# Optimization experiments

Measured on AMD Instinct MI355X. Metric: run time of the kernel, lower is better.

Reference implementation:

```python
import jax, jax.numpy as jnp
import numpy as np
import math

D_MODEL = 1024
N_HEADS = 16
D_HEAD = D_MODEL // N_HEADS


def _pos_encoding(seq_len, d_model):
    # matches get_pos_encoding: paired frequencies (repeat_interleave(2)),
    # sin on even columns, cos on odd columns of the SAME angle matrix.
    position = jnp.arange(seq_len, dtype=jnp.float32)[:, None]          # [L,1]
    div = 1.0 / (10000.0 ** (jnp.arange(0, d_model, 2, dtype=jnp.float32) / d_model))
    div = jnp.repeat(div, 2)[None, :]                                    # [1,D]
    ang = position * div                                                 # [L,D]
    col = jnp.arange(d_model)
    return jnp.where(col[None, :] % 2 == 0, jnp.sin(ang), jnp.cos(ang))


def _rel_enc_shift(a):
    # a: [b, h, l, m] -> Transformer-XL relative shift
    b, h, l, m = a.shape
    a = jnp.concatenate([a, jnp.zeros((b, h, l, 1), a.dtype)], axis=-1)  # [b,h,l,m+1]
    a = a.reshape(b, h, l * (m + 1))
    a = a[:, :, l - 1: l - 1 + l * m]
    return a.reshape(b, h, l, m)


def setup_inputs() -> dict:
    key = jax.random.key(0)
    ks = jax.random.split(key, 10)
    B, S, D = 1, 2048, D_MODEL
    s = 1.0 / math.sqrt(D)
    inp = {
        "query": jax.random.normal(ks[0], (B, S, D), jnp.float32),
        "key": jax.random.normal(ks[1], (B, S, D), jnp.float32),
        "value": jax.random.normal(ks[2], (B, S, D), jnp.float32),
        "attn_mask": jnp.zeros((1, 1, S, S), jnp.float32),
        "Wq": jax.random.normal(ks[3], (D, D), jnp.float32) * s,
        "Wke": jax.random.normal(ks[4], (D, D), jnp.float32) * s,
        "Wkr": jax.random.normal(ks[5], (D, D), jnp.float32) * s,
        "Wv": jax.random.normal(ks[6], (D, D), jnp.float32) * s,
        "Wf": jax.random.normal(ks[7], (D, D), jnp.float32) * s,
        "u_param": jax.random.normal(ks[8], (1, 1, N_HEADS, D_HEAD), jnp.float32),
        "v_param": jax.random.normal(ks[9], (1, 1, N_HEADS, D_HEAD), jnp.float32),
    }
    return inp


def reference(query, key, value, attn_mask, Wq, Wke, Wkr, Wv, Wf, u_param, v_param):
    B, S, D = query.shape
    F = key.shape[1]
    H, dh = u_param.shape[2], u_param.shape[3]
    sqrt_dk = math.sqrt(D)

    rel_enc = _pos_encoding(F, D)[::-1, :]                     # flipped along seq dim

    q = (query @ Wq.T).reshape(B, S, H, dh)
    k = (key @ Wke.T).reshape(B, F, H, dh)
    v = (value @ Wv.T).reshape(B, F, H, dh)

    A_C = jnp.einsum('bsnd,bfnd->bnsf', q + u_param, k)
    Q = (rel_enc @ Wkr.T).reshape(F, H, dh)
    B_D_hat = jnp.einsum('bsnd,fnd->bnsf', q + v_param, Q)
    B_D = _rel_enc_shift(B_D_hat)

    score = (A_C + B_D) / sqrt_dk + attn_mask
    weights = jax.nn.softmax(score, axis=-1)                   # [B,H,S,F]
    attention_loss = jnp.mean(jnp.max(weights, axis=(-1, -2)))

    out = jnp.einsum('bnsf,bfnd->bsnd', weights, v).reshape(B, S, D)
    out = jax.nn.gelu(out @ Wf.T, approximate=False)
    return out, weights, attention_loss
```

## Files before the change

kernel.cpp:

```cpp
#include <hip/hip_runtime.h>
#include <math.h>

#define SEQ 2048
#define DMODEL 1024
#define NHEADS 16
#define DHEAD 64

#define LSLOTS 64
#define LSTRIDE 32

typedef long long i64;
typedef unsigned short u16;
typedef __attribute__((ext_vector_type(4))) float f32x4;
typedef __attribute__((ext_vector_type(8))) short bf16x8;

#define IN_E  2097152
#define W_E   1048576
#define HEAD_E 131072

__device__ inline u16 f2bf(float x) {
    union { float f; unsigned u; } v; v.f = x;
    unsigned r = v.u + 0x7FFF + ((v.u >> 16) & 1);
    return (u16)(r >> 16);
}
__device__ inline float bf2f(u16 h) {
    union { unsigned u; float f; } v; v.u = ((unsigned)h) << 16;
    return v.f;
}

__device__ inline void gload16(const void* g, void* l) {
    __builtin_amdgcn_global_load_lds(
        (const __attribute__((address_space(1))) unsigned int*)g,
        (__attribute__((address_space(3))) unsigned int*)l, 16, 0, 0);
}

struct SplitArgs {
    const float* src[8];
    u16* dh[8];
    u16* dl[8];
    int n4[8];
};
__global__ __launch_bounds__(256)
void split_all(SplitArgs a)
{
    const int z = blockIdx.y;
    const int i = blockIdx.x * 256 + threadIdx.x;
    if (i >= a.n4[z]) return;
    const float4 x = ((const float4*)a.src[z])[i];
    u16 h0 = f2bf(x.x), h1 = f2bf(x.y), h2 = f2bf(x.z), h3 = f2bf(x.w);
    u16 l0 = f2bf(x.x - bf2f(h0)), l1 = f2bf(x.y - bf2f(h1));
    u16 l2 = f2bf(x.z - bf2f(h2)), l3 = f2bf(x.w - bf2f(h3));
    uint2 hh; hh.x = (unsigned)h0 | ((unsigned)h1 << 16); hh.y = (unsigned)h2 | ((unsigned)h3 << 16);
    uint2 ll; ll.x = (unsigned)l0 | ((unsigned)l1 << 16); ll.y = (unsigned)l2 | ((unsigned)l3 << 16);
    ((uint2*)a.dh[z])[i] = hh;
    ((uint2*)a.dl[z])[i] = ll;
}

__global__ __launch_bounds__(256)
void posenc_split(u16* __restrict__ dh, u16* __restrict__ dl)
{
    const int idx = blockIdx.x * 256 + threadIdx.x;
    const int f = idx >> 10;
    const int i = idx & 1023;
    const float P = (float)(SEQ - 1 - f);
    const float ex = (float)(i & ~1) * (1.f / 1024.f);
    const float dv = powf(10000.f, -ex);
    const float ang = P * dv;
    const float val = (i & 1) ? cosf(ang) : sinf(ang);
    const u16 hb = f2bf(val);
    dh[idx] = hb;
    dl[idx] = f2bf(val - bf2f(hb));
}

struct TNArgs {
    const u16 *Ah, *Al, *Bh, *Bl;
    i64 sAz, sBz;
    float* Cf; i64 sCz; int ldc;
    u16 *O1h, *O1l, *O2h, *O2l;
    const float *b1, *b2;
    int K, mode;
};

__global__ __launch_bounds__(256)
void mfma_tn128(TNArgs p)
{
    __shared__ __align__(16) u16 Ash[128 * 32];
    __shared__ __align__(16) u16 Asl[128 * 32];
    __shared__ __align__(16) u16 Bsh[128 * 32];
    __shared__ __align__(16) u16 Bsl[128 * 32];
    const int tid = threadIdx.x, wave = tid >> 6, lane = tid & 63;
    const int z = blockIdx.z;
    const i64 m0 = (i64)blockIdx.y * 128, n0 = (i64)blockIdx.x * 128;
    const int K = p.K;
    const u16* Abh = p.Ah + (i64)z * p.sAz;
    const u16* Abl = p.Al + (i64)z * p.sAz;
    const u16* Bbh = p.Bh + (i64)z * p.sBz;
    const u16* Bbl = p.Bl + (i64)z * p.sBz;
    const int r0 = tid >> 2, kc = (tid & 3) * 8;
    const int r1 = r0 + 64;
    u16* dA0 = &Ash[wave * 512];
    u16* dA1 = &Ash[2048 + wave * 512];
    u16* dA0l = &Asl[wave * 512];
    u16* dA1l = &Asl[2048 + wave * 512];
    u16* dB0 = &Bsh[wave * 512];
    u16* dB1 = &Bsh[2048 + wave * 512];
    u16* dB0l = &Bsl[wave * 512];
    u16* dB1l = &Bsl[2048 + wave * 512];
    const int wm = (wave >> 1) * 64, wn = (wave & 1) * 64;
    f32x4 acc[4][4] = {};

    for (int k0 = 0; k0 < K; k0 += 32) {
        __syncthreads();
        const i64 ga0 = (m0 + r0) * K + k0 + kc;
        const i64 ga1 = (m0 + r1) * K + k0 + kc;
        const i64 gb0 = (n0 + r0) * K + k0 + kc;
        const i64 gb1 = (n0 + r1) * K + k0 + kc;
        gload16(Abh + ga0, dA0);  gload16(Abh + ga1, dA1);
        gload16(Abl + ga0, dA0l); gload16(Abl + ga1, dA1l);
        gload16(Bbh + gb0, dB0);  gload16(Bbh + gb1, dB1);
        gload16(Bbl + gb0, dB0l); gload16(Bbl + gb1, dB1l);
        __syncthreads();
        const int fr = lane & 15, fk = (lane >> 4) * 8;
        bf16x8 fah[4], fal[4], fbh[4], fbl[4];
#pragma unroll
        for (int t = 0; t < 4; ++t) {
            fah[t] = *(const bf16x8*)&Ash[(wm + t * 16 + fr) * 32 + fk];
            fal[t] = *(const bf16x8*)&Asl[(wm + t * 16 + fr) * 32 + fk];
            fbh[t] = *(const bf16x8*)&Bsh[(wn + t * 16 + fr) * 32 + fk];
            fbl[t] = *(const bf16x8*)&Bsl[(wn + t * 16 + fr) * 32 + fk];
        }
#pragma unroll
        for (int mi = 0; mi < 4; ++mi)
#pragma unroll
            for (int ni = 0; ni < 4; ++ni) {
                acc[mi][ni] = __builtin_amdgcn_mfma_f32_16x16x32_bf16(fah[mi], fbh[ni], acc[mi][ni], 0, 0, 0);
                acc[mi][ni] = __builtin_amdgcn_mfma_f32_16x16x32_bf16(fah[mi], fbl[ni], acc[mi][ni], 0, 0, 0);
                acc[mi][ni] = __builtin_amdgcn_mfma_f32_16x16x32_bf16(fal[mi], fbh[ni], acc[mi][ni], 0, 0, 0);
            }
    }

    const int fr = lane & 15, fq = (lane >> 4) * 4;
    if (p.mode == 0) {
        float* C = p.Cf + (i64)z * p.sCz;
#pragma unroll
        for (int mi = 0; mi < 4; ++mi)
#pragma unroll
            for (int e = 0; e < 4; ++e) {
                const i64 row = m0 + wm + mi * 16 + fq + e;
#pragma unroll
                for (int ni = 0; ni < 4; ++ni)
                    C[row * p.ldc + n0 + wn + ni * 16 + fr] = acc[mi][ni][e];
            }
    } else if (p.mode == 3) {
        float* C = p.Cf + (i64)z * p.sCz;
#pragma unroll
        for (int mi = 0; mi < 4; ++mi)
#pragma unroll
            for (int e = 0; e < 4; ++e) {
                const int r = (int)(m0 + wm + mi * 16 + fq + e);
#pragma unroll
                for (int ni = 0; ni < 4; ++ni) {
                    const int f = (int)n0 + wn + ni * 16 + fr;
                    if (f >= SEQ - 1 - r)
                        C[(i64)r * SEQ + (f + r - (SEQ - 1))] = acc[mi][ni][e];
                    else if (r >= 1)
                        C[(i64)(r - 1) * SEQ + (f + r + 1)] = acc[mi][ni][e];
                }
            }
    } else if (p.mode == 1) {
        const i64 obase = (i64)z * IN_E;
#pragma unroll
        for (int mi = 0; mi < 4; ++mi)
#pragma unroll
            for (int e = 0; e < 4; ++e) {
                const i64 m = m0 + wm + mi * 16 + fq + e;
#pragma unroll
                for (int ni = 0; ni < 4; ++ni) {
                    const int c = (int)n0 + wn + ni * 16 + fr;
                    const int h = c >> 6, d = c & 63;
                    const i64 off = ((i64)h * SEQ + m) * DHEAD + d;
                    float v = acc[mi][ni][e];
                    if (z == 0) v += p.b1[c];
                    const u16 hb = f2bf(v);
                    const u16 lb = f2bf(v - bf2f(hb));
                    p.O1h[obase + off] = hb;
                    p.O1l[obase + off] = lb;
                    if (z == 0) {
                        const float v2 = acc[mi][ni][e] + p.b2[c];
                        const u16 hb2 = f2bf(v2);
                        const u16 lb2 = f2bf(v2 - bf2f(hb2));
                        p.O2h[off] = hb2;
                        p.O2l[off] = lb2;
                    }
                }
            }
    } else {
        float* C = p.Cf;
#pragma unroll
        for (int mi = 0; mi < 4; ++mi)
#pragma unroll
            for (int e = 0; e < 4; ++e) {
                const i64 row = m0 + wm + mi * 16 + fq + e;
#pragma unroll
                for (int ni = 0; ni < 4; ++ni) {
                    const float x = acc[mi][ni][e];
                    C[row * p.ldc + n0 + wn + ni * 16 + fr] =
                        0.5f * x * (1.f + erff(x * 0.70710678118654752f));
                }
            }
    }
}

__global__ __launch_bounds__(256)
void mfma_pv(const float* __restrict__ Wgt, const u16* __restrict__ VTh,
             const u16* __restrict__ VTl, u16* __restrict__ Oh, u16* __restrict__ Ol)
{
    __shared__ __align__(16) float Asf[256 * 32];
    __shared__ __align__(16) u16 Bsh[64 * 32];
    __shared__ __align__(16) u16 Bsl[64 * 32];
    const int tid = threadIdx.x, wave = tid >> 6, lane = tid & 63;
    const int z = blockIdx.z;
    const i64 m0 = (i64)blockIdx.y * 256;
    const float* A = Wgt + (i64)z * SEQ * SEQ;
    const u16* Bh = VTh + (i64)z * HEAD_E;
    const u16* Bl = VTl + (i64)z * HEAD_E;
    const int ar = tid >> 3, akc = (tid & 7) * 4;
    const int br = tid >> 2, bkc = (tid & 3) * 8;
    const int wm = wave * 64;
    f32x4 acc[4][4] = {};

    for (int k0 = 0; k0 < SEQ; k0 += 32) {
        __syncthreads();
#pragma unroll
        for (int i = 0; i < 8; ++i)
            gload16(A + (m0 + ar + i * 32) * SEQ + k0 + akc, &Asf[(i * 256 + wave * 64) * 4]);
        gload16(Bh + (i64)br * SEQ + k0 + bkc, &Bsh[wave * 512]);
        gload16(Bl + (i64)br * SEQ + k0 + bkc, &Bsl[wave * 512]);
        __syncthreads();
        const int fr = lane & 15, fk = (lane >> 4) * 8;
        bf16x8 fbh[4], fbl[4];
#pragma unroll
        for (int t = 0; t < 4; ++t) {
            fbh[t] = *(const bf16x8*)&Bsh[(t * 16 + fr) * 32 + fk];
            fbl[t] = *(const bf16x8*)&Bsl[(t * 16 + fr) * 32 + fk];
        }
#pragma unroll
        for (int mi = 0; mi < 4; ++mi) {
            const float4 x0 = *(const float4*)&Asf[(wm + mi * 16 + fr) * 32 + fk];
            const float4 x1 = *(const float4*)&Asf[(wm + mi * 16 + fr) * 32 + fk + 4];
            float av[8] = { x0.x, x0.y, x0.z, x0.w, x1.x, x1.y, x1.z, x1.w };
            bf16x8 ah, al;
#pragma unroll
            for (int j = 0; j < 8; ++j) {
                union { float f; unsigned u; } v; v.f = av[j];
                const u16 hb = (u16)(v.u >> 16);
                union { unsigned u; float f; } fh; fh.u = v.u & 0xFFFF0000u;
                union { float f; unsigned u; } rm; rm.f = av[j] - fh.f;
                ah[j] = (short)hb;
                al[j] = (short)(u16)(rm.u >> 16);
            }
#pragma unroll
            for (int ni = 0; ni < 4; ++ni) {
                acc[mi][ni] = __builtin_amdgcn_mfma_f32_16x16x32_bf16(ah, fbh[ni], acc[mi][ni], 0, 0, 0);
                acc[mi][ni] = __builtin_amdgcn_mfma_f32_16x16x32_bf16(ah, fbl[ni], acc[mi][ni], 0, 0, 0);
                acc[mi][ni] = __builtin_amdgcn_mfma_f32_16x16x32_bf16(al, fbh[ni], acc[mi][ni], 0, 0, 0);
            }
        }
    }

    const int fr = lane & 15, fq = (lane >> 4) * 4;
#pragma unroll
    for (int mi = 0; mi < 4; ++mi)
#pragma unroll
        for (int e = 0; e < 4; ++e) {
            const i64 m = m0 + wm + mi * 16 + fq + e;
#pragma unroll
            for (int ni = 0; ni < 4; ++ni) {
                const int c = z * 64 + ni * 16 + fr;
                const float v = acc[mi][ni][e];
                const u16 hb = f2bf(v);
                Oh[m * DMODEL + c] = hb;
                Ol[m * DMODEL + c] = f2bf(v - bf2f(hb));
            }
        }
}

__global__ __launch_bounds__(256)
void transpose_vv(const u16* __restrict__ vh, const u16* __restrict__ vl,
                  u16* __restrict__ th, u16* __restrict__ tl)
{
    __shared__ u16 tile[64][65];
    const int tid = threadIdx.x;
    const int h = blockIdx.y, f0 = blockIdx.x * 64;
    const i64 src = ((i64)h * SEQ + f0) * DHEAD;
    const i64 dst = (i64)h * HEAD_E + f0;
#pragma unroll
    for (int i = 0; i < 16; ++i) {
        const int idx = i * 256 + tid;
        const int r = idx >> 6, c = idx & 63;
        tile[c][r] = vh[src + (i64)r * 64 + c];
    }
    __syncthreads();
#pragma unroll
    for (int i = 0; i < 16; ++i) {
        const int idx = i * 256 + tid;
        const int d = idx >> 6, fl = idx & 63;
        th[dst + (i64)d * SEQ + fl] = tile[d][fl];
    }
    __syncthreads();
#pragma unroll
    for (int i = 0; i < 16; ++i) {
        const int idx = i * 256 + tid;
        const int r = idx >> 6, c = idx & 63;
        tile[c][r] = vl[src + (i64)r * 64 + c];
    }
    __syncthreads();
#pragma unroll
    for (int i = 0; i < 16; ++i) {
        const int idx = i * 256 + tid;
        const int d = idx >> 6, fl = idx & 63;
        tl[dst + (i64)d * SEQ + fl] = tile[d][fl];
    }
}

__global__ __launch_bounds__(256)
void softmax_rows(float* __restrict__ Wbase, const float* __restrict__ Gbase,
                  const float* __restrict__ mask, unsigned int* __restrict__ lmin, int h0)
{
    __shared__ float red[4];
    const int hl = blockIdx.y;
    float* Wh = Wbase + (i64)(h0 + hl) * SEQ * SEQ;
    const float* Gs = Gbase + (i64)hl * SEQ * SEQ;
    const int i = blockIdx.x;
    const int tx = threadIdx.x;
    const i64 rowoff = (i64)i * SEQ;
    float s[8];
    float mloc = -3.0e38f;
#pragma unroll
    for (int r = 0; r < 2; ++r) {
        const int j = (r << 10) + tx * 4;
        const float4 wv = *(const float4*)&Wh[rowoff + j];
        const float4 gv = *(const float4*)&Gs[rowoff + j];
        const float4 mk = *(const float4*)&mask[rowoff + j];
        const float wa[4] = { wv.x, wv.y, wv.z, wv.w };
        const float ga[4] = { gv.x, gv.y, gv.z, gv.w };
        const float ma[4] = { mk.x, mk.y, mk.z, mk.w };
#pragma unroll
        for (int e = 0; e < 4; ++e) {
            const float bd = (j + e == i + 1) ? 0.f : ga[e];
            const float v = (wa[e] + bd) * 0.03125f + ma[e];
            s[r * 4 + e] = v;
            mloc = fmaxf(mloc, v);
        }
    }
#pragma unroll
    for (int o = 32; o > 0; o >>= 1) mloc = fmaxf(mloc, __shfl_xor(mloc, o));
    if ((tx & 63) == 0) red[tx >> 6] = mloc;
    __syncthreads();
    const float m = fmaxf(fmaxf(red[0], red[1]), fmaxf(red[2], red[3]));
    __syncthreads();
    float lsum = 0.f;
#pragma unroll
    for (int r = 0; r < 8; ++r) { s[r] = __expf(s[r] - m); lsum += s[r]; }
#pragma unroll
    for (int o = 32; o > 0; o >>= 1) lsum += __shfl_xor(lsum, o);
    if ((tx & 63) == 0) red[tx >> 6] = lsum;
    __syncthreads();
    const float l = red[0] + red[1] + red[2] + red[3];
    const float inv = 1.f / l;
#pragma unroll
    for (int r = 0; r < 2; ++r) {
        const int j = (r << 10) + tx * 4;
        float4 ov;
        ov.x = s[r * 4 + 0] * inv;
        ov.y = s[r * 4 + 1] * inv;
        ov.z = s[r * 4 + 2] * inv;
        ov.w = s[r * 4 + 3] * inv;
        *(float4*)&Wh[rowoff + j] = ov;
    }
    if (tx == 0)
        atomicMin(&lmin[(((h0 + hl) << 6) + (i & (LSLOTS - 1))) * LSTRIDE],
                  __float_as_uint(l));
}

__global__ __launch_bounds__(1024)
void init_kernel(unsigned int* __restrict__ lmin)
{
    lmin[threadIdx.x * LSTRIDE] = 0x7F7FFFFFu;
}

__global__ __launch_bounds__(1024)
void loss_kernel(const unsigned int* __restrict__ lmin, float* __restrict__ out)
{
    __shared__ float hs[16];
    const int w = threadIdx.x >> 6;
    const int lane = threadIdx.x & 63;
    float l = __uint_as_float(lmin[threadIdx.x * LSTRIDE]);
#pragma unroll
    for (int o = 32; o > 0; o >>= 1) l = fminf(l, __shfl_xor(l, o));
    if (lane == 0) hs[w] = 1.f / l;
    __syncthreads();
    if (threadIdx.x == 0) {
        float v = 0.f;
#pragma unroll
        for (int h = 0; h < 16; ++h) v += hs[h];
        *out = v * (1.f / NHEADS);
    }
}

extern "C" void kernel_launch(void* const* d_in, const int* in_sizes, int n_in,
                              void* d_out, int out_size, void* d_ws, size_t ws_size,
                              hipStream_t stream)
{
    const float* query = (const float*)d_in[0];
    const float* key   = (const float*)d_in[1];
    const float* value = (const float*)d_in[2];
    const float* mask  = (const float*)d_in[3];
    const float* Wq    = (const float*)d_in[4];
    const float* Wke   = (const float*)d_in[5];
    const float* Wkr   = (const float*)d_in[6];
    const float* Wv    = (const float*)d_in[7];
    const float* Wf    = (const float*)d_in[8];
    const float* u_p   = (const float*)d_in[9];
    const float* v_p   = (const float*)d_in[10];

    float* out_final = (float*)d_out;
    float* weights   = out_final + (i64)SEQ * DMODEL;
    float* loss      = weights + (i64)NHEADS * SEQ * SEQ;

    char* w = (char*)d_ws;
    u16* in_h = (u16*)w;               w += (i64)4 * IN_E * 2;
    u16* in_l = (u16*)w;               w += (i64)4 * IN_E * 2;
    u16* W_h  = (u16*)w;               w += (i64)5 * W_E * 2;
    u16* W_l  = (u16*)w;               w += (i64)5 * W_E * 2;
    u16* P_h  = (u16*)w;               w += (i64)4 * IN_E * 2;
    u16* P_l  = (u16*)w;               w += (i64)4 * IN_E * 2;
    u16* qv_h = (u16*)w;               w += (i64)IN_E * 2;
    u16* qv_l = (u16*)w;               w += (i64)IN_E * 2;
    u16* vvT_h = (u16*)w;              w += (i64)IN_E * 2;
    u16* vvT_l = (u16*)w;              w += (i64)IN_E * 2;
    u16* o_h  = (u16*)w;               w += (i64)IN_E * 2;
    u16* o_l  = (u16*)w;               w += (i64)IN_E * 2;
    unsigned int* lmin = (unsigned int*)w; w += (i64)NHEADS * LSLOTS * LSTRIDE * 4;
    const i64 fixed_bytes = (i64)(w - (char*)d_ws);
    const i64 gbytes = (i64)SEQ * SEQ * 4;
    const i64 avail = (i64)ws_size - fixed_bytes;
    float* G;
    int chunk;
    if (avail >= gbytes) {
        G = (float*)w;
        i64 ch = avail / gbytes;
        chunk = ch > 16 ? 16 : (int)ch;
    } else {
        G = (float*)in_h;
        chunk = 2;
    }

    dim3 blk(256);
    init_kernel<<<dim3(1), dim3(1024), 0, stream>>>(lmin);

    SplitArgs sa;
    sa.src[0] = query; sa.dh[0] = in_h;           sa.dl[0] = in_l;           sa.n4[0] = IN_E / 4;
    sa.src[1] = key;   sa.dh[1] = in_h + IN_E;    sa.dl[1] = in_l + IN_E;    sa.n4[1] = IN_E / 4;
    sa.src[2] = value; sa.dh[2] = in_h + 2*IN_E;  sa.dl[2] = in_l + 2*IN_E;  sa.n4[2] = IN_E / 4;
    sa.src[3] = Wq;    sa.dh[3] = W_h;            sa.dl[3] = W_l;            sa.n4[3] = W_E / 4;
    sa.src[4] = Wke;   sa.dh[4] = W_h + W_E;      sa.dl[4] = W_l + W_E;      sa.n4[4] = W_E / 4;
    sa.src[5] = Wv;    sa.dh[5] = W_h + 2*W_E;    sa.dl[5] = W_l + 2*W_E;    sa.n4[5] = W_E / 4;
    sa.src[6] = Wkr;   sa.dh[6] = W_h + 3*W_E;    sa.dl[6] = W_l + 3*W_E;    sa.n4[6] = W_E / 4;
    sa.src[7] = Wf;    sa.dh[7] = W_h + 4*W_E;    sa.dl[7] = W_l + 4*W_E;    sa.n4[7] = W_E / 4;
    split_all<<<dim3(2048, 8), blk, 0, stream>>>(sa);
    posenc_split<<<dim3(IN_E / 256), blk, 0, stream>>>(in_h + 3*(i64)IN_E, in_l + 3*(i64)IN_E);

    {
        TNArgs p = {};
        p.Ah = in_h; p.Al = in_l; p.Bh = W_h; p.Bl = W_l;
        p.sAz = IN_E; p.sBz = W_E;
        p.O1h = P_h; p.O1l = P_l; p.O2h = qv_h; p.O2l = qv_l;
        p.b1 = u_p; p.b2 = v_p;
        p.K = DMODEL; p.mode = 1;
        mfma_tn128<<<dim3(DMODEL / 128, SEQ / 128, 4), blk, 0, stream>>>(p);
    }

    transpose_vv<<<dim3(SEQ / 64, NHEADS), blk, 0, stream>>>(
        P_h + 2*(i64)IN_E, P_l + 2*(i64)IN_E, vvT_h, vvT_l);

    {
        TNArgs p = {};
        p.Ah = P_h; p.Al = P_l;
        p.Bh = P_h + IN_E; p.Bl = P_l + IN_E;
        p.sAz = HEAD_E; p.sBz = HEAD_E;
        p.Cf = weights; p.sCz = (i64)SEQ * SEQ; p.ldc = SEQ;
        p.K = DHEAD; p.mode = 0;
        mfma_tn128<<<dim3(SEQ / 128, SEQ / 128, NHEADS), blk, 0, stream>>>(p);
    }

    for (int h0 = 0; h0 < NHEADS; h0 += chunk) {
        const int ch = (h0 + chunk <= NHEADS) ? chunk : (NHEADS - h0);
        TNArgs p = {};
        p.Ah = qv_h + (i64)h0 * HEAD_E; p.Al = qv_l + (i64)h0 * HEAD_E;
        p.Bh = P_h + 3*(i64)IN_E + (i64)h0 * HEAD_E;
        p.Bl = P_l + 3*(i64)IN_E + (i64)h0 * HEAD_E;
        p.sAz = HEAD_E; p.sBz = HEAD_E;
        p.Cf = G; p.sCz = (i64)SEQ * SEQ; p.ldc = SEQ;
        p.K = DHEAD; p.mode = 3;
        mfma_tn128<<<dim3(SEQ / 128, SEQ / 128, ch), blk, 0, stream>>>(p);
        softmax_rows<<<dim3(SEQ, ch), blk, 0, stream>>>(weights, G, mask, lmin, h0);
    }

    mfma_pv<<<dim3(1, SEQ / 256, NHEADS), blk, 0, stream>>>(weights, vvT_h, vvT_l, o_h, o_l);

    {
        TNArgs p = {};
        p.Ah = o_h; p.Al = o_l;
        p.Bh = W_h + 4*(i64)W_E; p.Bl = W_l + 4*(i64)W_E;
        p.sAz = 0; p.sBz = 0;
        p.Cf = out_final; p.sCz = 0; p.ldc = DMODEL;
        p.K = DMODEL; p.mode = 2;
        mfma_tn128<<<dim3(DMODEL / 128, SEQ / 128, 1), blk, 0, stream>>>(p);
    }

    loss_kernel<<<dim3(1), dim3(1024), 0, stream>>>(lmin, loss);
}
```

Baseline: 666.5 us.

## Fuse A_C GEMM with B_D, scale and mask into score buffer per chunk

The A_C GEMM now runs per head-chunk after the B_D GEMM and, in a new epilogue mode, reads the shifted B_D from the chunk buffer, adds its own result, scales, adds the mask and writes the final score in place. The B_D epilogue zeroes the diagonal+1 entry that the shift leaves unwritten, so softmax only loads one array instead of three. This drops the full-size A_C write into the weights buffer and two extra reads per softmax element. In exchange the A_C epilogue does a read-modify-write of G and a mask read, and the GEMM work is split into more launches.

```diff
diff --git a/kernel.cpp b/kernel.cpp
--- a/kernel.cpp
+++ b/kernel.cpp
@@ -78,6 +78,7 @@
     float* Cf; i64 sCz; int ldc;
     u16 *O1h, *O1l, *O2h, *O2l;
     const float *b1, *b2;
+    const float *msk;
     int K, mode;
 };
 
@@ -153,6 +154,10 @@
             }
     } else if (p.mode == 3) {
         float* C = p.Cf + (i64)z * p.sCz;
+        if (n0 == 0 && tid < 128) {
+            const int hr = (int)m0 + tid;
+            if (hr < SEQ - 1) C[(i64)hr * SEQ + hr + 1] = 0.f;
+        }
 #pragma unroll
         for (int mi = 0; mi < 4; ++mi)
 #pragma unroll
@@ -165,6 +170,21 @@
                         C[(i64)r * SEQ + (f + r - (SEQ - 1))] = acc[mi][ni][e];
                     else if (r >= 1)
                         C[(i64)(r - 1) * SEQ + (f + r + 1)] = acc[mi][ni][e];
+                }
+            }
+    } else if (p.mode == 5) {
+        float* C = p.Cf + (i64)z * p.sCz;
+        const float* M = p.msk;
+#pragma unroll
+        for (int mi = 0; mi < 4; ++mi)
+#pragma unroll
+            for (int e = 0; e < 4; ++e) {
+                const i64 row = m0 + wm + mi * 16 + fq + e;
+#pragma unroll
+                for (int ni = 0; ni < 4; ++ni) {
+                    const i64 idx = row * p.ldc + n0 + wn + ni * 16 + fr;
+                    C[idx] = (acc[mi][ni][e] + C[idx]) * 0.03125f
+                             + M[row * SEQ + n0 + wn + ni * 16 + fr];
                 }
             }
     } else if (p.mode == 1) {
@@ -324,13 +344,13 @@
 }
 
 __global__ __launch_bounds__(256)
-void softmax_rows(float* __restrict__ Wbase, const float* __restrict__ Gbase,
-                  const float* __restrict__ mask, unsigned int* __restrict__ lmin, int h0)
+void softmax_rows(float* __restrict__ Wbase, const float* __restrict__ Sbase,
+                  unsigned int* __restrict__ lmin, int h0)
 {
     __shared__ float red[4];
     const int hl = blockIdx.y;
     float* Wh = Wbase + (i64)(h0 + hl) * SEQ * SEQ;
-    const float* Gs = Gbase + (i64)hl * SEQ * SEQ;
+    const float* S = Sbase + (i64)hl * SEQ * SEQ;
     const int i = blockIdx.x;
     const int tx = threadIdx.x;
     const i64 rowoff = (i64)i * SEQ;
@@ -339,19 +359,10 @@
 #pragma unroll
     for (int r = 0; r < 2; ++r) {
         const int j = (r << 10) + tx * 4;
-        const float4 wv = *(const float4*)&Wh[rowoff + j];
-        const float4 gv = *(const float4*)&Gs[rowoff + j];
-        const float4 mk = *(const float4*)&mask[rowoff + j];
-        const float wa[4] = { wv.x, wv.y, wv.z, wv.w };
-        const float ga[4] = { gv.x, gv.y, gv.z, gv.w };
-        const float ma[4] = { mk.x, mk.y, mk.z, mk.w };
-#pragma unroll
-        for (int e = 0; e < 4; ++e) {
-            const float bd = (j + e == i + 1) ? 0.f : ga[e];
-            const float v = (wa[e] + bd) * 0.03125f + ma[e];
-            s[r * 4 + e] = v;
-            mloc = fmaxf(mloc, v);
-        }
+        const float4 sv = *(const float4*)&S[rowoff + j];
+        s[r * 4 + 0] = sv.x; s[r * 4 + 1] = sv.y;
+        s[r * 4 + 2] = sv.z; s[r * 4 + 3] = sv.w;
+        mloc = fmaxf(mloc, fmaxf(fmaxf(sv.x, sv.y), fmaxf(sv.z, sv.w)));
     }
 #pragma unroll
     for (int o = 32; o > 0; o >>= 1) mloc = fmaxf(mloc, __shfl_xor(mloc, o));
@@ -484,27 +495,29 @@
     transpose_vv<<<dim3(SEQ / 64, NHEADS), blk, 0, stream>>>(
         P_h + 2*(i64)IN_E, P_l + 2*(i64)IN_E, vvT_h, vvT_l);
 
-    {
-        TNArgs p = {};
-        p.Ah = P_h; p.Al = P_l;
-        p.Bh = P_h + IN_E; p.Bl = P_l + IN_E;
-        p.sAz = HEAD_E; p.sBz = HEAD_E;
-        p.Cf = weights; p.sCz = (i64)SEQ * SEQ; p.ldc = SEQ;
-        p.K = DHEAD; p.mode = 0;
-        mfma_tn128<<<dim3(SEQ / 128, SEQ / 128, NHEADS), blk, 0, stream>>>(p);
-    }
-
     for (int h0 = 0; h0 < NHEADS; h0 += chunk) {
         const int ch = (h0 + chunk <= NHEADS) ? chunk : (NHEADS - h0);
-        TNArgs p = {};
-        p.Ah = qv_h + (i64)h0 * HEAD_E; p.Al = qv_l + (i64)h0 * HEAD_E;
-        p.Bh = P_h + 3*(i64)IN_E + (i64)h0 * HEAD_E;
-        p.Bl = P_l + 3*(i64)IN_E + (i64)h0 * HEAD_E;
-        p.sAz = HEAD_E; p.sBz = HEAD_E;
-        p.Cf = G; p.sCz = (i64)SEQ * SEQ; p.ldc = SEQ;
-        p.K = DHEAD; p.mode = 3;
-        mfma_tn128<<<dim3(SEQ / 128, SEQ / 128, ch), blk, 0, stream>>>(p);
-        softmax_rows<<<dim3(SEQ, ch), blk, 0, stream>>>(weights, G, mask, lmin, h0);
+        {
+            TNArgs p = {};
+            p.Ah = qv_h + (i64)h0 * HEAD_E; p.Al = qv_l + (i64)h0 * HEAD_E;
+            p.Bh = P_h + 3*(i64)IN_E + (i64)h0 * HEAD_E;
+            p.Bl = P_l + 3*(i64)IN_E + (i64)h0 * HEAD_E;
+            p.sAz = HEAD_E; p.sBz = HEAD_E;
+            p.Cf = G; p.sCz = (i64)SEQ * SEQ; p.ldc = SEQ;
+            p.K = DHEAD; p.mode = 3;
+            mfma_tn128<<<dim3(SEQ / 128, SEQ / 128, ch), blk, 0, stream>>>(p);
+        }
+        {
+            TNArgs p = {};
+            p.Ah = P_h + (i64)h0 * HEAD_E; p.Al = P_l + (i64)h0 * HEAD_E;
+            p.Bh = P_h + IN_E + (i64)h0 * HEAD_E; p.Bl = P_l + IN_E + (i64)h0 * HEAD_E;
+            p.sAz = HEAD_E; p.sBz = HEAD_E;
+            p.Cf = G; p.sCz = (i64)SEQ * SEQ; p.ldc = SEQ;
+            p.msk = mask;
+            p.K = DHEAD; p.mode = 5;
+            mfma_tn128<<<dim3(SEQ / 128, SEQ / 128, ch), blk, 0, stream>>>(p);
+        }
+        softmax_rows<<<dim3(SEQ, ch), blk, 0, stream>>>(weights, G, lmin, h0);
     }
 
     mfma_pv<<<dim3(1, SEQ / 256, NHEADS), blk, 0, stream>>>(weights, vvT_h, vvT_l, o_h, o_l);
```

Result: slower. 737.8 us (+10.7%).
